# Optimization experiments

Measured on AMD Instinct MI355X. Metric: run time of the kernel, lower is better.

## Reference

```python
import jax, jax.numpy as jnp
import numpy as np

N_EVENT = 100000
N_TRACE = 20000
E_EE = 1000000
E_ET = 500000
E_TE = 500000
D = 128          # embedding_dim == hidden_dim
OUT = 64         # output_dim
L = 3            # num_layers
NTYPES_EDGES = 3 # edge types
B = 64           # graphs per batch


def setup_inputs() -> dict:
    key = jax.random.key(0)
    ks = jax.random.split(key, 16)
    s = 1.0 / np.sqrt(D)
    inp = {
        "event_ids": jnp.arange(N_EVENT, dtype=jnp.int64 if jax.config.jax_enable_x64 else jnp.int32),
        "trace_ids": jnp.arange(N_TRACE, dtype=jnp.int64 if jax.config.jax_enable_x64 else jnp.int32),
        "e2e_src": jax.random.randint(ks[0], (E_EE,), 0, N_EVENT),
        "e2e_dst": jax.random.randint(ks[1], (E_EE,), 0, N_EVENT),
        "e2t_src": jax.random.randint(ks[2], (E_ET,), 0, N_EVENT),
        "e2t_dst": jax.random.randint(ks[3], (E_ET,), 0, N_TRACE),
        "t2e_src": jax.random.randint(ks[4], (E_TE,), 0, N_TRACE),
        "t2e_dst": jax.random.randint(ks[5], (E_TE,), 0, N_EVENT),
        "event_batch": jnp.sort(jax.random.randint(ks[6], (N_EVENT,), 0, B)),
        "trace_batch": jnp.sort(jax.random.randint(ks[7], (N_TRACE,), 0, B)),
        # learned parameters
        "emb_event": jax.random.normal(ks[8], (N_EVENT, D), jnp.float32),
        "emb_trace": jax.random.normal(ks[9], (N_TRACE, D), jnp.float32),
        # per-layer, per-edge-type SAGEConv weights: lin_l (neighbor, with bias), lin_r (root, no bias)
        "Wl": jax.random.normal(ks[10], (L, NTYPES_EDGES, D, D), jnp.float32) * s,
        "bl": jnp.zeros((L, NTYPES_EDGES, D), jnp.float32),
        "Wr": jax.random.normal(ks[11], (L, NTYPES_EDGES, D, D), jnp.float32) * s,
        # output MLP head
        "W1": jax.random.normal(ks[12], (D, D), jnp.float32) * s,
        "b1": jnp.zeros((D,), jnp.float32),
        "W2": jax.random.normal(ks[13], (OUT, D), jnp.float32) * s,
        "b2": jnp.zeros((OUT,), jnp.float32),
    }
    return inp


def reference(event_ids, trace_ids, e2e_src, e2e_dst, e2t_src, e2t_dst,
              t2e_src, t2e_dst, event_batch, trace_batch,
              emb_event, emb_trace, Wl, bl, Wr, W1, b1, W2, b2):
    def seg_mean(x_src, src, dst, n_dst):
        # mean-aggregate source features onto destination nodes (SAGEConv default aggr)
        s = jax.ops.segment_sum(x_src[src], dst, num_segments=n_dst)
        c = jax.ops.segment_sum(jnp.ones(dst.shape, x_src.dtype), dst, num_segments=n_dst)
        return s / jnp.maximum(c, 1.0)[:, None]

    # per-node-type embedding lookup
    x = {"event": emb_event[event_ids], "trace": emb_trace[trace_ids]}
    n = {"event": event_ids.shape[0], "trace": trace_ids.shape[0]}
    # edge types: (src_type, dst_type, src_idx, dst_idx), conv index matches Wl/bl/Wr axis 1
    edges = [
        ("event", "event", e2e_src, e2e_dst),
        ("event", "trace", e2t_src, e2t_dst),
        ("trace", "event", t2e_src, t2e_dst),
    ]
    n_layers = Wl.shape[0]
    for l in range(n_layers):
        new = {k: jnp.zeros((n[k], Wl.shape[-2]), x[k].dtype) for k in x}
        for i, (st, dt, s_idx, d_idx) in enumerate(edges):
            m = seg_mean(x[st], s_idx, d_idx, n[dt])
            # SAGEConv: lin_l(mean neighbors) + lin_r(root); HeteroConv aggr='sum' across edge types
            new[dt] = new[dt] + m @ Wl[l, i].T + bl[l, i] + x[dt] @ Wr[l, i].T
        x = new
    # global_add_pool per node type, then stack+sum over node types
    pooled = (jax.ops.segment_sum(x["event"], event_batch, num_segments=B)
              + jax.ops.segment_sum(x["trace"], trace_batch, num_segments=B))
    h = jax.nn.relu(pooled @ W1.T + b1)
    return h @ W2.T + b2
```

## Files before the change

kernel.cpp:

```cpp
#include <hip/hip_runtime.h>
#include <hip/hip_bf16.h>


#define D 128
#define NB 64
#define OUTD 64
#define NLAY 3

typedef __bf16 bf16;
typedef __bf16 bf16x4 __attribute__((ext_vector_type(4)));
typedef __bf16 bf16x8 __attribute__((ext_vector_type(8)));
typedef float  f32x16 __attribute__((ext_vector_type(16)));

#define LOAD16_TO_LDS(gp, lp) \
    __builtin_amdgcn_global_load_lds((const __attribute__((address_space(1))) void*)(gp), \
                                     (__attribute__((address_space(3))) void*)(lp), 16, 0, 0)

__global__ void gather_all(const float* __restrict__ embE, const int* __restrict__ idsE,
                           bf16* __restrict__ xE, int nE,
                           const float* __restrict__ embT, const int* __restrict__ idsT,
                           bf16* __restrict__ xT, int nT) {
    int idx = blockIdx.x * blockDim.x + threadIdx.x;
    const float* emb; const int* ids; bf16* x;
    int tE = nE * 32;
    if (idx < tE) { emb = embE; ids = idsE; x = xE; }
    else {
        idx -= tE;
        if (idx >= nT * 32) return;
        emb = embT; ids = idsT; x = xT;
    }
    int r = idx >> 5, v = idx & 31;
    float4 f = ((const float4*)(emb + (size_t)ids[r] * D))[v];
    bf16x4 o;
    o[0] = (bf16)f.x; o[1] = (bf16)f.y; o[2] = (bf16)f.z; o[3] = (bf16)f.w;
    ((bf16x4*)(x + (size_t)r * D))[v] = o;
}

__global__ void hist_all(const int* __restrict__ dEE, const int* __restrict__ dET,
                         const int* __restrict__ dTE, int nEE, int nET, int nTE,
                         int* __restrict__ degEE, int* __restrict__ degET, int* __restrict__ degTE,
                         int* __restrict__ rkEE, int* __restrict__ rkET, int* __restrict__ rkTE) {
    int e = blockIdx.x * blockDim.x + threadIdx.x;
    const int* dst; int* deg; int* rk;
    if (e < nEE) { dst = dEE; deg = degEE; rk = rkEE; }
    else {
        e -= nEE;
        if (e < nET) { dst = dET; deg = degET; rk = rkET; }
        else {
            e -= nET;
            if (e >= nTE) return;
            dst = dTE; deg = degTE; rk = rkTE;
        }
    }
    rk[e] = atomicAdd(&deg[dst[e]], 1);
}

__global__ void scan_p1_all(const int* __restrict__ dA, int* __restrict__ oA, int* __restrict__ sA, int nA,
                            const int* __restrict__ dB, int* __restrict__ oB, int* __restrict__ sB, int nB,
                            const int* __restrict__ dC, int* __restrict__ oC, int* __restrict__ sC, int nC) {
    int nbA = (nA + 1023) >> 10, nbB = (nB + 1023) >> 10;
    int b = blockIdx.x;
    const int* deg; int* off; int* bsum; int n; int lb;
    if (b < nbA) { deg = dA; off = oA; bsum = sA; n = nA; lb = b; }
    else if (b < nbA + nbB) { deg = dB; off = oB; bsum = sB; n = nB; lb = b - nbA; }
    else { deg = dC; off = oC; bsum = sC; n = nC; lb = b - nbA - nbB; }
    __shared__ int s[256];
    int t = threadIdx.x;
    int base = lb * 1024 + t * 4;
    int v[4];
    #pragma unroll
    for (int i = 0; i < 4; ++i) v[i] = (base + i < n) ? deg[base + i] : 0;
    int tot = v[0] + v[1] + v[2] + v[3];
    s[t] = tot;
    __syncthreads();
    for (int st = 1; st < 256; st <<= 1) {
        int x = (t >= st) ? s[t - st] : 0;
        __syncthreads();
        s[t] += x;
        __syncthreads();
    }
    int run = s[t] - tot;
    #pragma unroll
    for (int i = 0; i < 4; ++i) {
        if (base + i < n) off[base + i] = run;
        run += v[i];
    }
    if (t == 255) bsum[lb] = s[255];
}

__global__ void scan_p2_all(int* __restrict__ sA, int nbA,
                            int* __restrict__ sB, int nbB,
                            int* __restrict__ sC, int nbC) {
    int* bsum; int nb;
    if (blockIdx.x == 0) { bsum = sA; nb = nbA; }
    else if (blockIdx.x == 1) { bsum = sB; nb = nbB; }
    else { bsum = sC; nb = nbC; }
    __shared__ int s[256];
    int t = threadIdx.x;
    int v = (t < nb) ? bsum[t] : 0;
    s[t] = v;
    __syncthreads();
    for (int st = 1; st < 256; st <<= 1) {
        int x = (t >= st) ? s[t - st] : 0;
        __syncthreads();
        s[t] += x;
        __syncthreads();
    }
    if (t < nb) bsum[t] = s[t] - v;
    if (t == 0) bsum[nb] = s[255];
}

__global__ void scan_p3_all(int* __restrict__ oA, const int* __restrict__ sA, int nA,
                            int* __restrict__ oB, const int* __restrict__ sB, int nB,
                            int* __restrict__ oC, const int* __restrict__ sC, int nC) {
    int cbA = (nA + 255) >> 8, cbB = (nB + 255) >> 8;
    int b = blockIdx.x;
    int* off; const int* bsum; int n; int lb;
    if (b < cbA) { off = oA; bsum = sA; n = nA; lb = b; }
    else if (b < cbA + cbB) { off = oB; bsum = sB; n = nB; lb = b - cbA; }
    else { off = oC; bsum = sC; n = nC; lb = b - cbA - cbB; }
    int i = lb * 256 + threadIdx.x;
    if (i < n) off[i] += bsum[i >> 10];
    if (i == 0) off[n] = bsum[(n + 1023) >> 10];
}

__global__ void adj_fill_all(const int* __restrict__ sEE, const int* __restrict__ dEE, int nEE,
                             const int* __restrict__ sET, const int* __restrict__ dET, int nET,
                             const int* __restrict__ sTE, const int* __restrict__ dTE, int nTE,
                             const int* __restrict__ oEE, const int* __restrict__ oET,
                             const int* __restrict__ oTE,
                             const int* __restrict__ rkEE, const int* __restrict__ rkET,
                             const int* __restrict__ rkTE,
                             int* __restrict__ adjEE, int* __restrict__ adjET,
                             int* __restrict__ adjTE) {
    int e = blockIdx.x * blockDim.x + threadIdx.x;
    const int* src; const int* dst; const int* off; const int* rk; int* adj;
    if (e < nEE) { src = sEE; dst = dEE; off = oEE; rk = rkEE; adj = adjEE; }
    else {
        e -= nEE;
        if (e < nET) { src = sET; dst = dET; off = oET; rk = rkET; adj = adjET; }
        else {
            e -= nET;
            if (e >= nTE) return;
            src = sTE; dst = dTE; off = oTE; rk = rkTE; adj = adjTE;
        }
    }
    __builtin_nontemporal_store(src[e], &adj[off[dst[e]] + rk[e]]);
}

__global__ void agg_all(const bf16* __restrict__ xE, const bf16* __restrict__ xT,
                        const int* __restrict__ offEE, const int* __restrict__ adjEE,
                        const int* __restrict__ offTE, const int* __restrict__ adjTE,
                        const int* __restrict__ offET, const int* __restrict__ adjET,
                        bf16* __restrict__ mEE, bf16* __restrict__ mTE, bf16* __restrict__ mET,
                        int nE, int nT) {
    int gw = (blockIdx.x * blockDim.x + threadIdx.x) >> 6;
    int lane = threadIdx.x & 63;
    int qE = (nE + 3) >> 2, qT = (nT + 3) >> 2;
    const bf16* xsrc; const int* off; const int* adj; bf16* out; int ndst;
    if (gw < qE) { xsrc = xE; off = offEE; adj = adjEE; out = mEE; ndst = nE; }
    else if (gw < 2 * qE) { gw -= qE; xsrc = xT; off = offTE; adj = adjTE; out = mTE; ndst = nE; }
    else {
        gw -= 2 * qE;
        if (gw >= qT) return;
        xsrc = xE; off = offET; adj = adjET; out = mET; ndst = nT;
    }
    int sub = lane >> 4;
    int sl  = lane & 15;
    int row = gw * 4 + sub;
    if (row >= ndst) row = ndst - 1;
    int s0 = off[row], s1 = off[row + 1];
    float a[8] = {};
    int j = s0;
    for (; j + 8 <= s1; j += 8) {
        int ii[8];
        #pragma unroll
        for (int u = 0; u < 8; ++u) ii[u] = adj[j + u];
        bf16x8 v[8];
        #pragma unroll
        for (int u = 0; u < 8; ++u) v[u] = ((const bf16x8*)(xsrc + (size_t)ii[u] * D))[sl];
        #pragma unroll
        for (int u = 0; u < 8; ++u)
            #pragma unroll
            for (int e = 0; e < 8; ++e) a[e] += (float)v[u][e];
    }
    for (; j + 4 <= s1; j += 4) {
        int i0 = adj[j], i1 = adj[j + 1], i2 = adj[j + 2], i3 = adj[j + 3];
        bf16x8 v0 = ((const bf16x8*)(xsrc + (size_t)i0 * D))[sl];
        bf16x8 v1 = ((const bf16x8*)(xsrc + (size_t)i1 * D))[sl];
        bf16x8 v2 = ((const bf16x8*)(xsrc + (size_t)i2 * D))[sl];
        bf16x8 v3 = ((const bf16x8*)(xsrc + (size_t)i3 * D))[sl];
        #pragma unroll
        for (int e = 0; e < 8; ++e)
            a[e] += (float)v0[e] + (float)v1[e] + (float)v2[e] + (float)v3[e];
    }
    for (; j < s1; ++j) {
        int i0 = adj[j];
        bf16x8 v0 = ((const bf16x8*)(xsrc + (size_t)i0 * D))[sl];
        #pragma unroll
        for (int e = 0; e < 8; ++e) a[e] += (float)v0[e];
    }
    float inv = 1.0f / fmaxf((float)(s1 - s0), 1.0f);
    bf16x8 o;
    #pragma unroll
    for (int e = 0; e < 8; ++e) o[e] = (bf16)(a[e] * inv);
    ((bf16x8*)(out + (size_t)row * D))[sl] = o;
}

__global__ void prep_weights_packed(const float* __restrict__ Wl, const float* __restrict__ Wr,
                                    bf16* __restrict__ wbuf) {
    int idx = blockIdx.x * blockDim.x + threadIdx.x;
    if (idx >= NLAY * 5 * 2048) return;
    int l = idx / (5 * 2048);
    int rem = idx - l * 5 * 2048;
    int mat = rem >> 11;
    int q = rem & 2047;
    int lane = q & 63, t = (q >> 6) & 7, w = q >> 9;
    int r = w * 32 + (lane & 31);
    int c = t * 16 + (lane >> 5) * 8;
    size_t l3 = (size_t)l * 3;
    const float* s0;
    const float* s1 = nullptr;
    switch (mat) {
        case 0: s0 = Wl + (l3 + 0) * D * D; break;
        case 1: s0 = Wl + (l3 + 2) * D * D; break;
        case 2: s0 = Wr + (l3 + 0) * D * D; s1 = Wr + (l3 + 2) * D * D; break;
        case 3: s0 = Wl + (l3 + 1) * D * D; break;
        default: s0 = Wr + (l3 + 1) * D * D; break;
    }
    bf16x8 hi, lo;
    #pragma unroll
    for (int e = 0; e < 8; ++e) {
        float v = s0[r * D + c + e];
        if (s1) v += s1[r * D + c + e];
        bf16 h = (bf16)v;
        hi[e] = h;
        lo[e] = (bf16)(v - (float)h);
    }
    bf16* base = wbuf + (size_t)l * 10 * D * D;
    ((bf16x8*)(base + (size_t)(2 * mat) * D * D))[q] = hi;
    ((bf16x8*)(base + (size_t)(2 * mat + 1) * D * D))[q] = lo;
}

__global__ void prep_bias(const float* __restrict__ bl, float* __restrict__ bbuf) {
    int idx = blockIdx.x * blockDim.x + threadIdx.x;
    if (idx >= NLAY * D) return;
    int l = idx >> 7, o = idx & (D - 1);
    bbuf[l * 2 * D + o]     = bl[(size_t)(l * 3 + 0) * D + o] + bl[(size_t)(l * 3 + 2) * D + o];
    bbuf[l * 2 * D + D + o] = bl[(size_t)(l * 3 + 1) * D + o];
}

__device__ __forceinline__ void gemm_body(const bf16* A0, const bf16* A1, const bf16* A2,
                                          const bf16* Wp, const float* bias, bf16* out,
                                          int M, int nm, int row0, bf16* As) {
    int tid = threadIdx.x;
    int wave = tid >> 6, lane = tid & 63;
    int m = lane & 31, half = lane >> 5;

    f32x16 acc[2];
    #pragma unroll
    for (int rt = 0; rt < 2; ++rt)
        #pragma unroll
        for (int i = 0; i < 16; ++i) acc[rt][i] = 0.f;

    const bf16* Aptr[3] = {A0, A1, A2};
    #pragma unroll
    for (int s = 0; s < 3; ++s) {
        if (s >= nm) break;
        if (s) __syncthreads();
        const bf16* Amat = Aptr[s];
        #pragma unroll
        for (int p = 0; p < 4; ++p) {
            int si = p * 256 + tid;
            int r = si >> 4, u = si & 15;
            int gr = row0 + r; if (gr >= M) gr = M - 1;
            int gc = (u ^ (r & 15)) * 8;
            LOAD16_TO_LDS(Amat + (size_t)gr * D + gc, As + (size_t)(p * 4 + wave) * 512);
        }
        const bf16* wph = Wp + (size_t)(2 * s) * D * D + ((size_t)wave * 512 + lane) * 8;
        const bf16* wpl = wph + D * D;
        bf16x8 bh_c  = *(const bf16x8*)(wph);
        bf16x8 blo_c = *(const bf16x8*)(wpl);
        __syncthreads();

        #pragma unroll 1
        for (int t = 0; t < 8; ++t) {
            bf16x8 bh_n, blo_n;
            if (t < 7) {
                bh_n  = *(const bf16x8*)(wph + (t + 1) * 512);
                blo_n = *(const bf16x8*)(wpl + (t + 1) * 512);
            }
            bf16x8 af[2];
            #pragma unroll
            for (int rt = 0; rt < 2; ++rt) {
                int r = rt * 32 + m;
                int c = t * 2 + half;
                af[rt] = *(const bf16x8*)(As + ((size_t)r * 16 + (c ^ (r & 15))) * 8);
            }
            acc[0] = __builtin_amdgcn_mfma_f32_32x32x16_bf16(af[0], bh_c,  acc[0], 0, 0, 0);
            acc[1] = __builtin_amdgcn_mfma_f32_32x32x16_bf16(af[1], bh_c,  acc[1], 0, 0, 0);
            acc[0] = __builtin_amdgcn_mfma_f32_32x32x16_bf16(af[0], blo_c, acc[0], 0, 0, 0);
            acc[1] = __builtin_amdgcn_mfma_f32_32x32x16_bf16(af[1], blo_c, acc[1], 0, 0, 0);
            bh_c = bh_n; blo_c = blo_n;
        }
    }

    int col = wave * 32 + m;
    float bv = bias[col];
    #pragma unroll
    for (int rt = 0; rt < 2; ++rt) {
        #pragma unroll
        for (int r = 0; r < 16; ++r) {
            int row = row0 + rt * 32 + (r & 3) + 8 * (r >> 2) + 4 * half;
            if (row < M) out[(size_t)row * D + col] = (bf16)(acc[rt][r] + bv);
        }
    }
}

__global__ __launch_bounds__(256) void gemm_all(const bf16* __restrict__ eA0, const bf16* __restrict__ eA1,
                                                const bf16* __restrict__ eA2, const bf16* __restrict__ eW,
                                                const float* __restrict__ eB, bf16* __restrict__ eOut,
                                                int Me, int bE,
                                                const bf16* __restrict__ tA0, const bf16* __restrict__ tA1,
                                                const bf16* __restrict__ tW, const float* __restrict__ tB,
                                                bf16* __restrict__ tOut, int Mt) {
    __shared__ bf16 As[64 * 128];
    if ((int)blockIdx.x < bE)
        gemm_body(eA0, eA1, eA2, eW, eB, eOut, Me, 3, blockIdx.x * 64, As);
    else
        gemm_body(tA0, tA1, (const bf16*)nullptr, tW, tB, tOut, Mt, 2,
                  ((int)blockIdx.x - bE) * 64, As);
}

__global__ void pool_m_all(const bf16* __restrict__ m_ee, const bf16* __restrict__ m_te,
                           const bf16* __restrict__ xE, const bf16* __restrict__ m_et,
                           const bf16* __restrict__ xT,
                           const int* __restrict__ bEv, const int* __restrict__ bTr,
                           int nE, int nT, int pbE, int pbT,
                           float* __restrict__ pooled5, int* __restrict__ cntE,
                           int* __restrict__ cntT) {
    int c = threadIdx.x;
    int blk = blockIdx.x;
    const bf16* x; const int* batch; int n, r0, s;
    if (blk < 3 * pbE) {
        s = blk / pbE; int lb = blk - s * pbE;
        x = (s == 0) ? m_ee : (s == 1) ? m_te : xE;
        batch = bEv; n = nE; r0 = lb * 64;
    } else {
        int q = blk - 3 * pbE;
        s = 3 + q / pbT; int lb = q - (s - 3) * pbT;
        x = (s == 3) ? m_et : xT;
        batch = bTr; n = nT; r0 = lb * 64;
    }
    int r1 = min(r0 + 64, n);
    if (r0 >= r1) return;
    float* P = pooled5 + (size_t)s * NB * D;
    int* cnt = (s == 2) ? cntE : (s == 4) ? cntT : nullptr;
    int cur = batch[r0];
    float acc = 0.f;
    int run = 0;
    for (int r = r0; r < r1; ++r) {
        int b = batch[r];
        if (b != cur) {
            atomicAdd(&P[cur * D + c], acc);
            if (cnt && c == 0) atomicAdd(&cnt[cur], run);
            acc = 0.f; run = 0; cur = b;
        }
        acc += (float)x[(size_t)r * D + c];
        run++;
    }
    atomicAdd(&P[cur * D + c], acc);
    if (cnt && c == 0) atomicAdd(&cnt[cur], run);
}

__global__ void tail_kernel(const float* __restrict__ pooled5, const int* __restrict__ cntE,
                            const int* __restrict__ cntT,
                            const float* __restrict__ Wl, const float* __restrict__ Wr,
                            const float* __restrict__ bl,
                            const float* __restrict__ W1, const float* __restrict__ b1,
                            const float* __restrict__ W2, const float* __restrict__ b2,
                            float* __restrict__ out) {
    __shared__ float p5[5][D];
    __shared__ float hp[D];
    __shared__ float hh[D];
    int b = blockIdx.x, t = threadIdx.x;
    #pragma unroll
    for (int s = 0; s < 5; ++s) p5[s][t] = pooled5[(size_t)(s * NB + b) * D + t];
    __syncthreads();
    float ce = (float)cntE[b], ct = (float)cntT[b];
    float s = ce * (bl[6 * D + t] + bl[8 * D + t]) + ct * bl[7 * D + t];
    const float* w0  = Wl + (size_t)6 * D * D + (size_t)t * D;
    const float* w2  = Wl + (size_t)8 * D * D + (size_t)t * D;
    const float* wr0 = Wr + (size_t)6 * D * D + (size_t)t * D;
    const float* wr2 = Wr + (size_t)8 * D * D + (size_t)t * D;
    const float* w1m = Wl + (size_t)7 * D * D + (size_t)t * D;
    const float* wr1 = Wr + (size_t)7 * D * D + (size_t)t * D;
    #pragma unroll 4
    for (int k = 0; k < D; ++k)
        s += p5[0][k] * w0[k] + p5[1][k] * w2[k] + p5[2][k] * (wr0[k] + wr2[k])
           + p5[3][k] * w1m[k] + p5[4][k] * wr1[k];
    hp[t] = s;
    __syncthreads();
    float s1 = b1[t];
    const float* u = W1 + (size_t)t * D;
    #pragma unroll 4
    for (int k = 0; k < D; ++k) s1 += hp[k] * u[k];
    hh[t] = fmaxf(s1, 0.f);
    __syncthreads();
    if (t < OUTD) {
        float s2 = b2[t];
        const float* v = W2 + (size_t)t * D;
        #pragma unroll 4
        for (int k = 0; k < D; ++k) s2 += hh[k] * v[k];
        out[b * OUTD + t] = s2;
    }
}

extern "C" void kernel_launch(void* const* d_in, const int* in_sizes, int n_in,
                              void* d_out, int out_size, void* d_ws, size_t ws_size,
                              hipStream_t stream) {
    const int* event_ids   = (const int*)d_in[0];
    const int* trace_ids   = (const int*)d_in[1];
    const int* e2e_src     = (const int*)d_in[2];
    const int* e2e_dst     = (const int*)d_in[3];
    const int* e2t_src     = (const int*)d_in[4];
    const int* e2t_dst     = (const int*)d_in[5];
    const int* t2e_src     = (const int*)d_in[6];
    const int* t2e_dst     = (const int*)d_in[7];
    const int* event_batch = (const int*)d_in[8];
    const int* trace_batch = (const int*)d_in[9];
    const float* emb_event = (const float*)d_in[10];
    const float* emb_trace = (const float*)d_in[11];
    const float* Wl        = (const float*)d_in[12];
    const float* bl        = (const float*)d_in[13];
    const float* Wr        = (const float*)d_in[14];
    const float* W1        = (const float*)d_in[15];
    const float* b1        = (const float*)d_in[16];
    const float* W2        = (const float*)d_in[17];
    const float* b2        = (const float*)d_in[18];

    const int NE = in_sizes[0];
    const int NT = in_sizes[1];
    const int EE = in_sizes[2];
    const int ET = in_sizes[4];
    const int TE = in_sizes[6];

    size_t cur = 0;
    auto alloc = [&](size_t bytes) -> void* {
        cur = (cur + 255) & ~(size_t)255;
        void* p = (char*)d_ws + cur;
        cur += bytes;
        return p;
    };
    bf16* x_event   = (bf16*)alloc((size_t)NE * D * 2);
    bf16* x_trace   = (bf16*)alloc((size_t)NT * D * 2);
    bf16* nx_event  = (bf16*)alloc((size_t)NE * D * 2);
    bf16* nx_trace  = (bf16*)alloc((size_t)NT * D * 2);
    bf16* m_ee      = (bf16*)alloc((size_t)NE * D * 2);
    bf16* m_te      = (bf16*)alloc((size_t)NE * D * 2);
    bf16* m_et      = (bf16*)alloc((size_t)NT * D * 2);
    bf16* wbuf      = (bf16*)alloc((size_t)NLAY * 10 * D * D * 2);
    float* bbuf     = (float*)alloc((size_t)NLAY * 2 * D * 4);
    size_t zInts = (size_t)NE + NT + NE + 5 * NB * D + 2 * NB;
    int* zbase  = (int*)alloc(zInts * 4);
    int* deg_ee = zbase;
    int* deg_et = deg_ee + NE;
    int* deg_te = deg_et + NT;
    float* pooled5 = (float*)(deg_te + NE);
    int* cntE = (int*)(pooled5 + 5 * NB * D);
    int* cntT = cntE + NB;
    int* off_ee = (int*)alloc((size_t)(NE + 1) * 4);
    int* adj_ee = (int*)alloc((size_t)EE * 4);
    int* off_et = (int*)alloc((size_t)(NT + 1) * 4);
    int* adj_et = (int*)alloc((size_t)ET * 4);
    int* off_te = (int*)alloc((size_t)(NE + 1) * 4);
    int* adj_te = (int*)alloc((size_t)TE * 4);
    int* bsum_ee = (int*)alloc(((size_t)(NE + 1023) / 1024 + 1) * 4);
    int* bsum_et = (int*)alloc(((size_t)(NT + 1023) / 1024 + 1) * 4);
    int* bsum_te = (int*)alloc(((size_t)(NE + 1023) / 1024 + 1) * 4);
    int* rk_ee = (int*)m_ee;
    int* rk_et = (int*)m_te;
    int* rk_te = (int*)m_et;
    (void)ws_size; (void)n_in; (void)out_size;

    const int nbE = (NE + 1023) / 1024;
    const int nbT = (NT + 1023) / 1024;

    hipMemsetAsync(zbase, 0, zInts * 4, stream);

    gather_all<<<((NE + NT) * 32 + 255) / 256, 256, 0, stream>>>(
        emb_event, event_ids, x_event, NE, emb_trace, trace_ids, x_trace, NT);

    prep_weights_packed<<<(NLAY * 5 * 2048 + 255) / 256, 256, 0, stream>>>(Wl, Wr, wbuf);
    prep_bias<<<(NLAY * D + 255) / 256, 256, 0, stream>>>(bl, bbuf);

    hist_all<<<(EE + ET + TE + 255) / 256, 256, 0, stream>>>(
        e2e_dst, e2t_dst, t2e_dst, EE, ET, TE,
        deg_ee, deg_et, deg_te, rk_ee, rk_et, rk_te);
    scan_p1_all<<<nbE + nbT + nbE, 256, 0, stream>>>(
        deg_ee, off_ee, bsum_ee, NE, deg_et, off_et, bsum_et, NT, deg_te, off_te, bsum_te, NE);
    scan_p2_all<<<3, 256, 0, stream>>>(bsum_ee, nbE, bsum_et, nbT, bsum_te, nbE);
    scan_p3_all<<<((NE + 255) >> 8) * 2 + ((NT + 255) >> 8), 256, 0, stream>>>(
        off_ee, bsum_ee, NE, off_et, bsum_et, NT, off_te, bsum_te, NE);
    adj_fill_all<<<(EE + ET + TE + 255) / 256, 256, 0, stream>>>(
        e2e_src, e2e_dst, EE, e2t_src, e2t_dst, ET, t2e_src, t2e_dst, TE,
        off_ee, off_et, off_te, rk_ee, rk_et, rk_te, adj_ee, adj_et, adj_te);

    const int qE = (NE + 3) >> 2, qT = (NT + 3) >> 2;
    const int aggBlocks = (2 * qE + qT + 3) / 4;
    const int bE = (NE + 63) / 64, bT = (NT + 63) / 64;
    for (int l = 0; l < NLAY; ++l) {
        agg_all<<<aggBlocks, 256, 0, stream>>>(x_event, x_trace,
                                               off_ee, adj_ee, off_te, adj_te, off_et, adj_et,
                                               m_ee, m_te, m_et, NE, NT);
        if (l < NLAY - 1) {
            const bf16* wl_ev = wbuf + (size_t)l * 10 * D * D;
            const bf16* wl_tr = wl_ev + (size_t)6 * D * D;
            const float* be = bbuf + (size_t)l * 2 * D;
            const float* bt = be + D;
            gemm_all<<<bE + bT, 256, 0, stream>>>(m_ee, m_te, x_event, wl_ev, be, nx_event, NE, bE,
                                                  m_et, x_trace, wl_tr, bt, nx_trace, NT);
            bf16* t;
            t = x_event; x_event = nx_event; nx_event = t;
            t = x_trace; x_trace = nx_trace; nx_trace = t;
        }
    }

    const int pbE = (NE + 63) / 64, pbT = (NT + 63) / 64;
    pool_m_all<<<3 * pbE + 2 * pbT, D, 0, stream>>>(m_ee, m_te, x_event, m_et, x_trace,
                                                    event_batch, trace_batch, NE, NT, pbE, pbT,
                                                    pooled5, cntE, cntT);
    tail_kernel<<<NB, D, 0, stream>>>(pooled5, cntE, cntT, Wl, Wr, bl,
                                      W1, b1, W2, b2, (float*)d_out);
}
```

Before: 684.0 us.

## Build CSR via two-level bucket sort with LDS atomics instead of global atomics

Replaces the global-atomic degree histogram and rank-based adjacency fill with a bucketed counting sort. Edges are first binned into 512-destination buckets using per-block LDS histograms, scanned, and scattered as (src,dst) pairs. A per-bucket kernel then builds offsets and adjacency using LDS atomics. The aim is to cut contended global atomics and random scattered writes, at the cost of an extra pass and extra intermediate traffic. It also reuses the message buffers as scratch and shrinks the memset.

Measured after the change: 602.3 us. 11.9% less time.

```diff
diff --git a/kernel.cpp b/kernel.cpp
--- a/kernel.cpp
+++ b/kernel.cpp
@@ -6,6 +6,8 @@
 #define NB 64
 #define OUTD 64
 #define NLAY 3
+#define EPB 4096
+#define BSH2 9
 
 typedef __bf16 bf16;
 typedef __bf16 bf16x4 __attribute__((ext_vector_type(4)));
@@ -36,23 +38,24 @@
     ((bf16x4*)(x + (size_t)r * D))[v] = o;
 }
 
-__global__ void hist_all(const int* __restrict__ dEE, const int* __restrict__ dET,
-                         const int* __restrict__ dTE, int nEE, int nET, int nTE,
-                         int* __restrict__ degEE, int* __restrict__ degET, int* __restrict__ degTE,
-                         int* __restrict__ rkEE, int* __restrict__ rkET, int* __restrict__ rkTE) {
-    int e = blockIdx.x * blockDim.x + threadIdx.x;
-    const int* dst; int* deg; int* rk;
-    if (e < nEE) { dst = dEE; deg = degEE; rk = rkEE; }
-    else {
-        e -= nEE;
-        if (e < nET) { dst = dET; deg = degET; rk = rkET; }
-        else {
-            e -= nET;
-            if (e >= nTE) return;
-            dst = dTE; deg = degTE; rk = rkTE;
-        }
-    }
-    rk[e] = atomicAdd(&deg[dst[e]], 1);
+__global__ void bkt_hist_all(const int* __restrict__ dEE, int nEE, int nbkEE, int nblkEE,
+                             int* __restrict__ cntEE,
+                             const int* __restrict__ dET, int nET, int nbkET, int nblkET,
+                             int* __restrict__ cntET,
+                             const int* __restrict__ dTE, int nTE, int nbkTE, int nblkTE,
+                             int* __restrict__ cntTE) {
+    __shared__ int h[256];
+    int b = blockIdx.x;
+    const int* dst; int E, nbk, nblk, lb; int* cnt;
+    if (b < nblkEE) { dst = dEE; E = nEE; nbk = nbkEE; nblk = nblkEE; cnt = cntEE; lb = b; }
+    else if (b < nblkEE + nblkET) { dst = dET; E = nET; nbk = nbkET; nblk = nblkET; cnt = cntET; lb = b - nblkEE; }
+    else { dst = dTE; E = nTE; nbk = nbkTE; nblk = nblkTE; cnt = cntTE; lb = b - nblkEE - nblkET; }
+    h[threadIdx.x] = 0;
+    __syncthreads();
+    int e0 = lb * EPB, e1 = min(e0 + EPB, E);
+    for (int e = e0 + threadIdx.x; e < e1; e += 256) atomicAdd(&h[dst[e] >> BSH2], 1);
+    __syncthreads();
+    for (int k = threadIdx.x; k < nbk; k += 256) cnt[k * nblk + lb] = h[k];
 }
 
 __global__ void scan_p1_all(const int* __restrict__ dA, int* __restrict__ oA, int* __restrict__ sA, int nA,
@@ -124,28 +127,78 @@
     if (i == 0) off[n] = bsum[(n + 1023) >> 10];
 }
 
-__global__ void adj_fill_all(const int* __restrict__ sEE, const int* __restrict__ dEE, int nEE,
-                             const int* __restrict__ sET, const int* __restrict__ dET, int nET,
-                             const int* __restrict__ sTE, const int* __restrict__ dTE, int nTE,
-                             const int* __restrict__ oEE, const int* __restrict__ oET,
-                             const int* __restrict__ oTE,
-                             const int* __restrict__ rkEE, const int* __restrict__ rkET,
-                             const int* __restrict__ rkTE,
-                             int* __restrict__ adjEE, int* __restrict__ adjET,
-                             int* __restrict__ adjTE) {
-    int e = blockIdx.x * blockDim.x + threadIdx.x;
-    const int* src; const int* dst; const int* off; const int* rk; int* adj;
-    if (e < nEE) { src = sEE; dst = dEE; off = oEE; rk = rkEE; adj = adjEE; }
-    else {
-        e -= nEE;
-        if (e < nET) { src = sET; dst = dET; off = oET; rk = rkET; adj = adjET; }
-        else {
-            e -= nET;
-            if (e >= nTE) return;
-            src = sTE; dst = dTE; off = oTE; rk = rkTE; adj = adjTE;
-        }
-    }
-    __builtin_nontemporal_store(src[e], &adj[off[dst[e]] + rk[e]]);
+__global__ void bkt_scatter_all(const int* __restrict__ sEE, const int* __restrict__ dEE,
+                                int nEE, int nbkEE, int nblkEE, const int* __restrict__ SEE,
+                                int2* __restrict__ ebEE,
+                                const int* __restrict__ sET, const int* __restrict__ dET,
+                                int nET, int nbkET, int nblkET, const int* __restrict__ SET,
+                                int2* __restrict__ ebET,
+                                const int* __restrict__ sTE, const int* __restrict__ dTE,
+                                int nTE, int nbkTE, int nblkTE, const int* __restrict__ STE,
+                                int2* __restrict__ ebTE) {
+    __shared__ int cu[256];
+    int b = blockIdx.x;
+    const int* src; const int* dst; const int* S; int2* eb; int E, nbk, nblk, lb;
+    if (b < nblkEE) { src = sEE; dst = dEE; S = SEE; eb = ebEE; E = nEE; nbk = nbkEE; nblk = nblkEE; lb = b; }
+    else if (b < nblkEE + nblkET) { src = sET; dst = dET; S = SET; eb = ebET; E = nET; nbk = nbkET; nblk = nblkET; lb = b - nblkEE; }
+    else { src = sTE; dst = dTE; S = STE; eb = ebTE; E = nTE; nbk = nbkTE; nblk = nblkTE; lb = b - nblkEE - nblkET; }
+    for (int k = threadIdx.x; k < nbk; k += 256) cu[k] = S[k * nblk + lb];
+    __syncthreads();
+    int e0 = lb * EPB, e1 = min(e0 + EPB, E);
+    for (int e = e0 + threadIdx.x; e < e1; e += 256) {
+        int s = src[e], d = dst[e];
+        int p = atomicAdd(&cu[d >> BSH2], 1);
+        eb[p] = make_int2(s, d);
+    }
+}
+
+__global__ void csr_build_all(const int2* __restrict__ ebEE, const int* __restrict__ SEE,
+                              int nbkEE, int nblkEE, int ndEE,
+                              int* __restrict__ offEE, int* __restrict__ adjEE,
+                              const int2* __restrict__ ebET, const int* __restrict__ SET,
+                              int nbkET, int nblkET, int ndET,
+                              int* __restrict__ offET, int* __restrict__ adjET,
+                              const int2* __restrict__ ebTE, const int* __restrict__ STE,
+                              int nbkTE, int nblkTE, int ndTE,
+                              int* __restrict__ offTE, int* __restrict__ adjTE) {
+    __shared__ int h[512];
+    __shared__ int ps[256];
+    __shared__ int cc[512];
+    int b = blockIdx.x;
+    const int2* eb; const int* S; int nbk, nblk, ndst, k; int* off; int* adj;
+    if (b < nbkEE) { eb = ebEE; S = SEE; nbk = nbkEE; nblk = nblkEE; ndst = ndEE; off = offEE; adj = adjEE; k = b; }
+    else if (b < nbkEE + nbkET) { eb = ebET; S = SET; nbk = nbkET; nblk = nblkET; ndst = ndET; off = offET; adj = adjET; k = b - nbkEE; }
+    else { eb = ebTE; S = STE; nbk = nbkTE; nblk = nblkTE; ndst = ndTE; off = offTE; adj = adjTE; k = b - nbkEE - nbkET; }
+    int base = S[k * nblk];
+    int end  = (k == nbk - 1) ? S[nbk * nblk] : S[(k + 1) * nblk];
+    int d0 = k << BSH2;
+    int t = threadIdx.x;
+    h[t] = 0; h[t + 256] = 0;
+    __syncthreads();
+    for (int j = base + t; j < end; j += 256) atomicAdd(&h[eb[j].y - d0], 1);
+    __syncthreads();
+    int a0 = h[2 * t], a1 = h[2 * t + 1];
+    ps[t] = a0 + a1;
+    __syncthreads();
+    for (int st = 1; st < 256; st <<= 1) {
+        int x = (t >= st) ? ps[t - st] : 0;
+        __syncthreads();
+        ps[t] += x;
+        __syncthreads();
+    }
+    int pe = ps[t] - (a0 + a1);
+    int o0 = base + pe, o1 = base + pe + a0;
+    cc[2 * t] = o0; cc[2 * t + 1] = o1;
+    int nd = min(512, ndst - d0);
+    if (2 * t < nd) off[d0 + 2 * t] = o0;
+    if (2 * t + 1 < nd) off[d0 + 2 * t + 1] = o1;
+    if (t == 0 && k == nbk - 1) off[ndst] = end;
+    __syncthreads();
+    for (int j = base + t; j < end; j += 256) {
+        int2 e = eb[j];
+        int p = atomicAdd(&cc[e.y - d0], 1);
+        adj[p] = e.x;
+    }
 }
 
 __global__ void agg_all(const bf16* __restrict__ xE, const bf16* __restrict__ xT,
@@ -445,6 +498,11 @@
     const int ET = in_sizes[4];
     const int TE = in_sizes[6];
 
+    const int nbkEE = (NE + 511) >> BSH2, nblkEE = (EE + EPB - 1) / EPB;
+    const int nbkET = (NT + 511) >> BSH2, nblkET = (ET + EPB - 1) / EPB;
+    const int nbkTE = (NE + 511) >> BSH2, nblkTE = (TE + EPB - 1) / EPB;
+    const int cEE = nbkEE * nblkEE, cET = nbkET * nblkET, cTE = nbkTE * nblkTE;
+
     size_t cur = 0;
     auto alloc = [&](size_t bytes) -> void* {
         cur = (cur + 255) & ~(size_t)255;
@@ -461,12 +519,9 @@
     bf16* m_et      = (bf16*)alloc((size_t)NT * D * 2);
     bf16* wbuf      = (bf16*)alloc((size_t)NLAY * 10 * D * D * 2);
     float* bbuf     = (float*)alloc((size_t)NLAY * 2 * D * 4);
-    size_t zInts = (size_t)NE + NT + NE + 5 * NB * D + 2 * NB;
+    size_t zInts = (size_t)5 * NB * D + 2 * NB;
     int* zbase  = (int*)alloc(zInts * 4);
-    int* deg_ee = zbase;
-    int* deg_et = deg_ee + NE;
-    int* deg_te = deg_et + NT;
-    float* pooled5 = (float*)(deg_te + NE);
+    float* pooled5 = (float*)zbase;
     int* cntE = (int*)(pooled5 + 5 * NB * D);
     int* cntT = cntE + NB;
     int* off_ee = (int*)alloc((size_t)(NE + 1) * 4);
@@ -475,16 +530,19 @@
     int* adj_et = (int*)alloc((size_t)ET * 4);
     int* off_te = (int*)alloc((size_t)(NE + 1) * 4);
     int* adj_te = (int*)alloc((size_t)TE * 4);
-    int* bsum_ee = (int*)alloc(((size_t)(NE + 1023) / 1024 + 1) * 4);
-    int* bsum_et = (int*)alloc(((size_t)(NT + 1023) / 1024 + 1) * 4);
-    int* bsum_te = (int*)alloc(((size_t)(NE + 1023) / 1024 + 1) * 4);
-    int* rk_ee = (int*)m_ee;
-    int* rk_et = (int*)m_te;
-    int* rk_te = (int*)m_et;
+    int* cnt_ee = (int*)alloc((size_t)cEE * 4);
+    int* S_ee   = (int*)alloc((size_t)(cEE + 1) * 4);
+    int* cnt_et = (int*)alloc((size_t)cET * 4);
+    int* S_et   = (int*)alloc((size_t)(cET + 1) * 4);
+    int* cnt_te = (int*)alloc((size_t)cTE * 4);
+    int* S_te   = (int*)alloc((size_t)(cTE + 1) * 4);
+    int* bsum_ee = (int*)alloc(((size_t)(cEE + 1023) / 1024 + 1) * 4);
+    int* bsum_et = (int*)alloc(((size_t)(cET + 1023) / 1024 + 1) * 4);
+    int* bsum_te = (int*)alloc(((size_t)(cTE + 1023) / 1024 + 1) * 4);
+    int2* eb_ee = (int2*)m_ee;
+    int2* eb_et = (int2*)m_te;
+    int2* eb_te = (int2*)m_et;
     (void)ws_size; (void)n_in; (void)out_size;
-
-    const int nbE = (NE + 1023) / 1024;
-    const int nbT = (NT + 1023) / 1024;
 
     hipMemsetAsync(zbase, 0, zInts * 4, stream);
 
@@ -494,17 +552,24 @@
     prep_weights_packed<<<(NLAY * 5 * 2048 + 255) / 256, 256, 0, stream>>>(Wl, Wr, wbuf);
     prep_bias<<<(NLAY * D + 255) / 256, 256, 0, stream>>>(bl, bbuf);
 
-    hist_all<<<(EE + ET + TE + 255) / 256, 256, 0, stream>>>(
-        e2e_dst, e2t_dst, t2e_dst, EE, ET, TE,
-        deg_ee, deg_et, deg_te, rk_ee, rk_et, rk_te);
-    scan_p1_all<<<nbE + nbT + nbE, 256, 0, stream>>>(
-        deg_ee, off_ee, bsum_ee, NE, deg_et, off_et, bsum_et, NT, deg_te, off_te, bsum_te, NE);
-    scan_p2_all<<<3, 256, 0, stream>>>(bsum_ee, nbE, bsum_et, nbT, bsum_te, nbE);
-    scan_p3_all<<<((NE + 255) >> 8) * 2 + ((NT + 255) >> 8), 256, 0, stream>>>(
-        off_ee, bsum_ee, NE, off_et, bsum_et, NT, off_te, bsum_te, NE);
-    adj_fill_all<<<(EE + ET + TE + 255) / 256, 256, 0, stream>>>(
-        e2e_src, e2e_dst, EE, e2t_src, e2t_dst, ET, t2e_src, t2e_dst, TE,
-        off_ee, off_et, off_te, rk_ee, rk_et, rk_te, adj_ee, adj_et, adj_te);
+    bkt_hist_all<<<nblkEE + nblkET + nblkTE, 256, 0, stream>>>(
+        e2e_dst, EE, nbkEE, nblkEE, cnt_ee,
+        e2t_dst, ET, nbkET, nblkET, cnt_et,
+        t2e_dst, TE, nbkTE, nblkTE, cnt_te);
+    const int nb1 = (cEE + 1023) >> 10, nb2 = (cET + 1023) >> 10, nb3 = (cTE + 1023) >> 10;
+    scan_p1_all<<<nb1 + nb2 + nb3, 256, 0, stream>>>(
+        cnt_ee, S_ee, bsum_ee, cEE, cnt_et, S_et, bsum_et, cET, cnt_te, S_te, bsum_te, cTE);
+    scan_p2_all<<<3, 256, 0, stream>>>(bsum_ee, nb1, bsum_et, nb2, bsum_te, nb3);
+    scan_p3_all<<<((cEE + 255) >> 8) + ((cET + 255) >> 8) + ((cTE + 255) >> 8), 256, 0, stream>>>(
+        S_ee, bsum_ee, cEE, S_et, bsum_et, cET, S_te, bsum_te, cTE);
+    bkt_scatter_all<<<nblkEE + nblkET + nblkTE, 256, 0, stream>>>(
+        e2e_src, e2e_dst, EE, nbkEE, nblkEE, S_ee, eb_ee,
+        e2t_src, e2t_dst, ET, nbkET, nblkET, S_et, eb_et,
+        t2e_src, t2e_dst, TE, nbkTE, nblkTE, S_te, eb_te);
+    csr_build_all<<<nbkEE + nbkET + nbkTE, 256, 0, stream>>>(
+        eb_ee, S_ee, nbkEE, nblkEE, NE, off_ee, adj_ee,
+        eb_et, S_et, nbkET, nblkET, NT, off_et, adj_et,
+        eb_te, S_te, nbkTE, nblkTE, NE, off_te, adj_te);
 
     const int qE = (NE + 3) >> 2, qT = (NT + 3) >> 2;
     const int aggBlocks = (2 * qE + qT + 3) / 4;
```
